# Kernel optimization log

Measured on AMD Instinct MI355X. Metric: run time of the kernel, lower is better.

Reference implementation:

```python
import jax, jax.numpy as jnp
import numpy as np
from jax import lax

B, DIM, H, W = 32, 256, 64, 64
DS = DIM // 4          # dim_split = 64
MLP_H = int(DIM * 2.0)  # mlp_ratio = 2.0
AK = 11                 # att_kernel
EPS = 1e-5


def conv(x, w, b=None, padding=(0, 0), dilation=1, groups=1, stride=1):
    y = lax.conv_general_dilated(
        x, w, (stride, stride),
        [(padding[0], padding[0]), (padding[1], padding[1])],
        rhs_dilation=(dilation, dilation),
        dimension_numbers=('NCHW', 'OIHW', 'NCHW'),
        feature_group_count=groups)
    if b is not None:
        y = y + b[None, :, None, None]
    return y


def bn(x):
    # BatchNorm2d, training-mode batch stats, affine at default init (gamma=1, beta=0)
    m = x.mean(axis=(0, 2, 3), keepdims=True)
    v = ((x - m) ** 2).mean(axis=(0, 2, 3), keepdims=True)
    return (x - m) * lax.rsqrt(v + EPS)


def maxpool2x2(x):
    b, c, h, w = x.shape
    xw = x.reshape(b, c, h // 2, 2, w // 2, 2).transpose(0, 1, 2, 4, 3, 5).reshape(b, c, h // 2, w // 2, 4)
    return xw.max(axis=-1), jnp.argmax(xw, axis=-1)


def maxunpool2x2(y, idx):
    b, c, h, w = y.shape
    oh = jax.nn.one_hot(idx, 4, dtype=y.dtype)  # scatter back into 2x2 window argmax slot
    out = (y[..., None] * oh).reshape(b, c, h, w, 2, 2).transpose(0, 1, 2, 4, 3, 5)
    return out.reshape(b, c, 2 * h, 2 * w)


def maxpool3(x):
    return lax.reduce_window(x, -jnp.inf, lax.max, (1, 1, 3, 3), (1, 1, 1, 1),
                             [(0, 0), (0, 0), (1, 1), (1, 1)])


def blurpool(x):
    # antialiased_cnns.BlurPool(C, stride=3): filt_size=4, reflect pad (1,2)
    f = jnp.array([1., 3., 3., 1.], dtype=x.dtype)
    k = f[:, None] * f[None, :]
    k = k / k.sum()
    c = x.shape[1]
    wgt = jnp.broadcast_to(k[None, None], (c, 1, 4, 4))
    xp = jnp.pad(x, ((0, 0), (0, 0), (1, 2), (1, 2)), mode='reflect')
    return lax.conv_general_dilated(xp, wgt, (3, 3), [(0, 0), (0, 0)],
                                    dimension_numbers=('NCHW', 'OIHW', 'NCHW'),
                                    feature_group_count=c)


def h_tf(x):
    b, c, hh, ww = x.shape
    x = jnp.pad(x, ((0, 0), (0, 0), (0, 0), (0, ww)))
    x = x.reshape(b, c, -1)[..., :-ww]
    return x.reshape(b, c, hh, 2 * ww - 1)


def inv_h_tf(x):
    b, c, hh, _ = x.shape
    x = x.reshape(b, c, -1)
    x = jnp.pad(x, ((0, 0), (0, 0), (0, hh)))
    return x.reshape(b, c, hh, 2 * hh)[..., :hh]


def v_tf(x):
    return h_tf(x.transpose(0, 1, 3, 2)).transpose(0, 1, 3, 2)


def inv_v_tf(x):
    return inv_h_tf(x.transpose(0, 1, 3, 2)).transpose(0, 1, 3, 2)


def ga12(x, p1w, p1b, c0w, c0b, spw, spb, c1w, c1b, c2w, c2b, cw, cb, sqw, sqb, p2w, p2b):
    xp, idx = maxpool2x2(x)
    c = xp.shape[1]
    h = jax.nn.relu(conv(xp, p1w, p1b))
    a1 = conv(h, c0w, c0b, padding=(2, 2), groups=c)                 # depthwise 5x5
    a2 = conv(a1, spw, spb, padding=(9, 9), dilation=3, groups=c)    # depthwise 7x7 dil3
    a1s = conv(a1, c1w, c1b)
    a2s = conv(a2, c2w, c2b)
    comb = jnp.concatenate([a1s, a2s], axis=1)
    agg = jnp.concatenate([comb.mean(axis=1, keepdims=True),
                           comb.max(axis=1, keepdims=True)], axis=1)
    sig = jax.nn.sigmoid(conv(agg, sqw, sqb, padding=(3, 3)))
    attn = conv(a1s * sig[:, 0:1] + a2s * sig[:, 1:2], cw, cb)
    h = conv(h * attn, p2w, p2b)
    return maxunpool2x2(h, idx)


def setup_inputs() -> dict:
    key = jax.random.key(0)
    ks = jax.random.split(key, 32)
    r = lambda i, shape: jax.random.normal(ks[i], shape, jnp.float32) * 0.05
    return {
        'x': jax.random.normal(ks[0], (B, DIM, H, W), jnp.float32),
        'pa_w1': r(1, (4 * DS, DS, 1, 1)),
        'pa_w2': r(2, (DS, 4 * DS, 1, 1)),
        'la_w': r(3, (DS, DS, 3, 3)),
        'mra_h1': r(4, (DS, 1, AK, 3)),
        'mra_v1': r(5, (DS, 1, 3, AK)),
        'mra_h2': r(6, (DS, 1, AK, 3)),
        'mra_v2': r(7, (DS, 1, 3, AK)),
        'g_proj1_w': r(8, (DS, DS, 1, 1)), 'g_proj1_b': r(9, (DS,)),
        'g_conv0_w': r(10, (DS, 1, 5, 5)), 'g_conv0_b': r(11, (DS,)),
        'g_sp_w': r(12, (DS, 1, 7, 7)), 'g_sp_b': r(13, (DS,)),
        'g_c1_w': r(14, (DS // 2, DS, 1, 1)), 'g_c1_b': r(15, (DS // 2,)),
        'g_c2_w': r(16, (DS // 2, DS, 1, 1)), 'g_c2_b': r(17, (DS // 2,)),
        'g_c_w': r(18, (DS, DS // 2, 1, 1)), 'g_c_b': r(19, (DS,)),
        'g_sq_w': r(20, (2, 2, 7, 7)), 'g_sq_b': r(21, (2,)),
        'g_proj2_w': r(22, (DS, DS, 1, 1)), 'g_proj2_b': r(23, (DS,)),
        'mlp_w1': r(24, (MLP_H, DIM, 1, 1)),
        'mlp_w2': r(25, (DIM, MLP_H, 1, 1)),
    }


def reference(x, pa_w1, pa_w2, la_w, mra_h1, mra_v1, mra_h2, mra_v2,
              g_proj1_w, g_proj1_b, g_conv0_w, g_conv0_b, g_sp_w, g_sp_b,
              g_c1_w, g_c1_b, g_c2_w, g_c2_b, g_c_w, g_c_b,
              g_sq_w, g_sq_b, g_proj2_w, g_proj2_b, mlp_w1, mlp_w2):
    x1, x2, x3, x4 = jnp.split(x, 4, axis=1)
    # PA: pixel attention (1x1 expand -> BN -> ReLU -> 1x1) sigmoid gate
    xa1 = x1 * jax.nn.sigmoid(conv(jax.nn.relu(bn(conv(x1, pa_w1))), pa_w2))
    # LA: 3x3 conv -> BN -> ReLU
    xa2 = jax.nn.relu(bn(conv(x2, la_w, padding=(1, 1))))
    # MRA: maxpool3x3 -> blurpool(stride3) -> 4 strip depthwise convs (+diag shear) -> BN -> sigmoid -> nearest upsample gate
    xm = blurpool(maxpool3(x3))
    ph, pv = (AK // 2, 1), (1, AK // 2)
    xh1 = conv(xm, mra_h1, padding=ph, groups=DS)
    xw1 = conv(xm, mra_v1, padding=pv, groups=DS)
    xh2 = inv_h_tf(conv(h_tf(xm), mra_h2, padding=ph, groups=DS))
    xw2 = inv_v_tf(conv(v_tf(xm), mra_v2, padding=pv, groups=DS))
    gate = jax.nn.sigmoid(bn(xh1 + xw1 + xh2 + xw2))
    hs, ws = gate.shape[-2:]
    ri = (jnp.arange(H) * hs) // H   # torch F.interpolate mode='nearest' index rule
    ci = (jnp.arange(W) * ws) // W
    xa3 = x3 * gate[:, :, ri][:, :, :, ci]
    # D_GA (stage==2): maxpool -> GA12 -> BN -> maxunpool
    x4p, idx1 = maxpool2x2(x4)
    xg = ga12(x4p, g_proj1_w, g_proj1_b, g_conv0_w, g_conv0_b, g_sp_w, g_sp_b,
              g_c1_w, g_c1_b, g_c2_w, g_c2_b, g_c_w, g_c_b, g_sq_w, g_sq_b,
              g_proj2_w, g_proj2_b)
    xa4 = maxunpool2x2(bn(xg), idx1)
    x_att = jnp.concatenate([xa1, xa2, xa3, xa4], axis=1)
    # residual MLP (drop_path=0 -> identity)
    return x + conv(jax.nn.relu(bn(conv(x_att, mlp_w1))), mlp_w2)
```

## Files before the change

kernel.cpp:

```cpp
#include <hip/hip_runtime.h>
#include <hip/hip_bf16.h>
#include <math.h>

typedef __hip_bfloat16 bf16;
typedef __attribute__((ext_vector_type(4))) float f32x4;
typedef __attribute__((ext_vector_type(8))) short s16x8;
typedef __attribute__((ext_vector_type(4))) short s16x4;

static __device__ __forceinline__ float bits2f(short s){ return __uint_as_float(((unsigned)(unsigned short)s)<<16); }
static __device__ __forceinline__ short bfbits(float f){ bf16 h = __float2bfloat16(f); return *reinterpret_cast<short*>(&h); }
static __device__ __forceinline__ float ldf(float v){ return v; }
static __device__ __forceinline__ float sigm(float v){ return 1.f/(1.f+__expf(-v)); }

#define P_IMG 4096

#define GLDS16(SRC, DST) __builtin_amdgcn_global_load_lds( \
    (__attribute__((address_space(1))) void*)(SRC), \
    (__attribute__((address_space(3))) void*)(DST), 16, 0, 0)

namespace {
constexpr long long XATT_OFF = 0;
constexpr long long BIG_OFF  = 67108864;
constexpr long long MISC     = 134217728;
constexpr long long XM_OFF   = MISC;
constexpr long long MSUM_OFF = MISC + 3964928;
constexpr long long X4P_OFF  = MISC + 23429120;
constexpr long long IDX1_OFF = MISC + 31817728;
constexpr long long XP_OFF   = MISC + 40206336;
constexpr long long IDX2_OFF = MISC + 42303488;
constexpr long long HBUF_OFF = MISC + 44400640;
constexpr long long A1_OFF   = MISC + 46497792;
constexpr long long A2_OFF   = MISC + 48594944;
constexpr long long A1S_OFF  = MISC + 50692096;
constexpr long long A2S_OFF  = MISC + 51740672;
constexpr long long AGG_OFF  = MISC + 52789248;
constexpr long long SIG_OFF  = MISC + 52854784;
constexpr long long ATTN_OFF = MISC + 52920320;
constexpr long long H2_OFF   = MISC + 55017472;
constexpr long long XG_OFF   = MISC + 57114624;
constexpr long long P33_OFF  = 201326592;
constexpr long long STATS_OFF= 234881024;
constexpr long long WS_NEED  = 234897408;
constexpr long long XPM_OFF  = MISC;
constexpr long long YLA_OFF  = MISC + 33554432;
}

__global__ __launch_bounds__(256) void zero_out_k(float* __restrict__ o, int n){
    int i = blockIdx.x*256 + threadIdx.x;
    if (i < n) o[i] = 0.f;
}

__global__ __launch_bounds__(256) void packw_k(const float* __restrict__ W, short* __restrict__ Wp,
                                               int kshift, int OT16)
{
    int i = blockIdx.x*256 + threadIdx.x;
    int o = i >> kshift;
    int k = i & ((1<<kshift)-1);
    long dest = (((((long)(k>>6)*2 + ((k>>5)&1))*OT16 + (o>>4))*4 + ((k>>3)&3))*16 + (o&15))*8 + (k&7);
    Wp[dest] = bfbits(W[i]);
}

__global__ __launch_bounds__(256) void packw_la_k(const float* __restrict__ W, short* __restrict__ Wp)
{
    int i = blockIdx.x*256 + threadIdx.x;
    int o = i / 576, k = i - o*576;
    int tap = k >> 6, c = k & 63;
    long dest = (((((long)(k>>6)*2 + ((k>>5)&1))*4 + (o>>4))*4 + ((k>>3)&3))*16 + (o&15))*8 + (k&7);
    Wp[dest] = bfbits(W[(o*64 + c)*9 + tap]);
}

__global__ __launch_bounds__(256) void xpose_pm_k(const float* __restrict__ x, short* __restrict__ xpm)
{
    int i = blockIdx.x*256 + threadIdx.x;
    int px = i & 4095, og = (i >> 12) & 15, b = i >> 16;
    s16x8 ov;
    #pragma unroll
    for (int j=0;j<8;j++)
        ov[j] = bfbits(x[((long)b*256 + og*8 + j)*P_IMG + px]);
    *(s16x8*)&xpm[((long)b*P_IMG + px)*128 + og*8] = ov;
}

template<int MT>
__global__ __launch_bounds__(256) void convmfma_dma_k(
    const short* __restrict__ in, int inCtot, int inOff,
    const short* __restrict__ Wp, int K, int OT16,
    short* __restrict__ out, int outC)
{
    static_assert(MT == 4 || MT == 8, "vmcnt counts assume MT in {4,8}");
    __shared__ __align__(16) short sB[2][64*64];
    const int tid = threadIdx.x;
    const int b = blockIdx.z;
    const int Mbase = blockIdx.y * (32*MT);
    const int pxBase = blockIdx.x * 64;
    const int lane = tid & 63, w = tid >> 6;
    const int n16 = lane & 15, q = lane >> 4;
    const int wm = w >> 1, wn = w & 1;
    const int otBase = (Mbase>>4) + wm*MT;

    f32x4 zero = {0.f,0.f,0.f,0.f};
    f32x4 acc[MT][2];
    #pragma unroll
    for (int mt=0;mt<MT;mt++){ acc[mt][0]=zero; acc[mt][1]=zero; }

    const int drow_lo = lane >> 3;
    const int chunk = lane & 7;
    const int seg0 = w*2, seg1 = w*2 + 1;
    const int row0 = seg0*8 + drow_lo, row1 = seg1*8 + drow_lo;
    const int kg0 = chunk ^ (row0 & 7), kg1 = chunk ^ (row1 & 7);
    const short* src0 = in + ((long)b*P_IMG + pxBase + row0)*inCtot + inOff + kg0*8;
    const short* src1 = in + ((long)b*P_IMG + pxBase + row1)*inCtot + inOff + kg1*8;

    const int NT = K >> 6;
    GLDS16(src0, (char*)&sB[0][0] + seg0*1024);
    GLDS16(src1, (char*)&sB[0][0] + seg1*1024);

    for (int t = 0; t < NT; t++){
        const int kb = t << 6;
        s16x8 afr[2][MT];
        #pragma unroll
        for (int kk=0; kk<2; kk++)
            #pragma unroll
            for (int mt=0; mt<MT; mt++)
                afr[kk][mt] = *(const s16x8*)(Wp + ((((long)t*2 + kk)*OT16 + otBase + mt)*64 + lane)*8);
        __builtin_amdgcn_sched_barrier(0);
        if (t+1 < NT){
            GLDS16(src0 + kb + 64, (char*)&sB[(t+1)&1][0] + seg0*1024);
            GLDS16(src1 + kb + 64, (char*)&sB[(t+1)&1][0] + seg1*1024);
            __builtin_amdgcn_sched_barrier(0);
            if constexpr (MT == 8) asm volatile("s_waitcnt vmcnt(18)" ::: "memory");
            else                   asm volatile("s_waitcnt vmcnt(10)" ::: "memory");
        } else {
            __builtin_amdgcn_sched_barrier(0);
            if constexpr (MT == 8) asm volatile("s_waitcnt vmcnt(16)" ::: "memory");
            else                   asm volatile("s_waitcnt vmcnt(8)" ::: "memory");
        }
        __builtin_amdgcn_sched_barrier(0);
        __builtin_amdgcn_s_barrier();
        __builtin_amdgcn_sched_barrier(0);
        const short* sC = &sB[t&1][0];
        #pragma unroll
        for (int kk = 0; kk < 2; kk++){
            s16x8 bfr[2];
            #pragma unroll
            for (int nt=0; nt<2; nt++){
                int n = wn*32 + nt*16 + n16;
                int g = (kk*4 + q) ^ (n & 7);
                bfr[nt] = *(const s16x8*)&sC[n*64 + (g<<3)];
            }
            #pragma unroll
            for (int mt=0; mt<MT; mt++)
                #pragma unroll
                for (int nt=0; nt<2; nt++)
                    acc[mt][nt] = __builtin_amdgcn_mfma_f32_16x16x32_bf16(afr[kk][mt], bfr[nt], acc[mt][nt], 0, 0, 0);
        }
        __builtin_amdgcn_sched_barrier(0);
        __builtin_amdgcn_s_barrier();
        __builtin_amdgcn_sched_barrier(0);
    }

    #pragma unroll
    for (int mt=0; mt<MT; mt++){
        #pragma unroll
        for (int nt=0; nt<2; nt++){
            int px = pxBase + wn*32 + nt*16 + n16;
            int o0 = Mbase + wm*(MT*16) + mt*16 + q*4;
            s16x4 ov;
            #pragma unroll
            for (int r=0; r<4; r++) ov[r] = bfbits(acc[mt][nt][r]);
            *(s16x4*)&out[((long)b*P_IMG + px)*outC + o0] = ov;
        }
    }
}

__global__ __launch_bounds__(256) void la_mfma_k(
    const short* __restrict__ xpm,
    const short* __restrict__ Wp,
    short* __restrict__ y)
{
    __shared__ __align__(16) short sB[2][64*64];
    const int tid = threadIdx.x;
    const int b = blockIdx.z;
    const int hRow = blockIdx.x;
    const int pxBase = hRow*64;
    const int lane = tid & 63, w = tid >> 6;
    const int n16 = lane & 15, q = lane >> 4;
    const int wm = w >> 1, wn = w & 1;
    const int otBase = wm*2;

    f32x4 zero = {0.f,0.f,0.f,0.f};
    f32x4 acc[2][2];
    acc[0][0]=zero; acc[0][1]=zero; acc[1][0]=zero; acc[1][1]=zero;

    const int srow = tid >> 3, schunk = tid & 7;
    const int kgA = schunk ^ (srow & 7);

    auto tapload = [&](int tap, s16x8& v0, s16x8& v1){
        int hh = hRow + (tap/3) - 1;
        int dw = (tap%3) - 1;
        bool hok = (unsigned)hh < 64u;
        s16x8 z = {0,0,0,0,0,0,0,0};
        v0 = z; v1 = z;
        int w0 = srow + dw, w1 = 32 + srow + dw;
        if (hok && (unsigned)w0 < 64u)
            v0 = *(const s16x8*)(xpm + ((long)b*P_IMG + hh*64 + w0)*128 + 64 + kgA*8);
        if (hok && (unsigned)w1 < 64u)
            v1 = *(const s16x8*)(xpm + ((long)b*P_IMG + hh*64 + w1)*128 + 64 + kgA*8);
    };

    s16x8 cv0, cv1;
    tapload(0, cv0, cv1);

    for (int tap = 0; tap < 9; tap++){
        s16x8 nv0 = cv0, nv1 = cv1;
        if (tap+1 < 9) tapload(tap+1, nv0, nv1);
        *(s16x8*)&sB[tap&1][srow*64 + schunk*8]      = cv0;
        *(s16x8*)&sB[tap&1][(32+srow)*64 + schunk*8] = cv1;
        asm volatile("s_waitcnt lgkmcnt(0)" ::: "memory");
        __builtin_amdgcn_sched_barrier(0);
        __builtin_amdgcn_s_barrier();
        __builtin_amdgcn_sched_barrier(0);
        const short* sC = &sB[tap&1][0];
        #pragma unroll
        for (int kk = 0; kk < 2; kk++){
            s16x8 afr[2], bfr[2];
            #pragma unroll
            for (int mt=0; mt<2; mt++)
                afr[mt] = *(const s16x8*)(Wp + ((((long)tap*2 + kk)*4 + otBase + mt)*64 + lane)*8);
            #pragma unroll
            for (int nt=0; nt<2; nt++){
                int n = wn*32 + nt*16 + n16;
                int g = (kk*4 + q) ^ (n & 7);
                bfr[nt] = *(const s16x8*)&sC[n*64 + (g<<3)];
            }
            #pragma unroll
            for (int mt=0; mt<2; mt++)
                #pragma unroll
                for (int nt=0; nt<2; nt++)
                    acc[mt][nt] = __builtin_amdgcn_mfma_f32_16x16x32_bf16(afr[mt], bfr[nt], acc[mt][nt], 0, 0, 0);
        }
        __builtin_amdgcn_sched_barrier(0);
        __builtin_amdgcn_s_barrier();
        __builtin_amdgcn_sched_barrier(0);
        cv0 = nv0; cv1 = nv1;
    }

    #pragma unroll
    for (int mt=0; mt<2; mt++){
        #pragma unroll
        for (int nt=0; nt<2; nt++){
            int px = pxBase + wn*32 + nt*16 + n16;
            int o0 = wm*32 + mt*16 + q*4;
            s16x4 ov;
            #pragma unroll
            for (int r=0; r<4; r++) ov[r] = bfbits(acc[mt][nt][r]);
            *(s16x4*)&y[((long)b*P_IMG + px)*64 + o0] = ov;
        }
    }
}

template<int EPI, typename TOUT, int MT>
__global__ __launch_bounds__(256) void convmfma_reg_k(
    const short* __restrict__ in, int inCtot, int inOff,
    const float2* __restrict__ stats,
    const short* __restrict__ Wp, int K, int OT16,
    TOUT* __restrict__ out, int outC, int outOff,
    const float* __restrict__ aux, int auxC, int auxOff)
{
    __shared__ __align__(16) short sB[2][64*64];
    const int tid = threadIdx.x;
    const int b = blockIdx.z;
    const int Mbase = blockIdx.y * (32*MT);
    const int pxBase = blockIdx.x * 64;
    const int lane = tid & 63, w = tid >> 6;
    const int n16 = lane & 15, q = lane >> 4;
    const int wm = w >> 1, wn = w & 1;
    const int otBase = (Mbase>>4) + wm*MT;

    f32x4 zero = {0.f,0.f,0.f,0.f};
    f32x4 acc[MT][2];
    #pragma unroll
    for (int mt=0;mt<MT;mt++){ acc[mt][0]=zero; acc[mt][1]=zero; }

    const int srow = tid >> 3, schunk = tid & 7;
    const int skg = schunk ^ (srow & 7);
    const short* inrow0 = in + ((long)b*P_IMG + pxBase + srow)*inCtot + inOff + skg*8;
    const short* inrow1 = in + ((long)b*P_IMG + pxBase + 32 + srow)*inCtot + inOff + skg*8;
    const float2* stp = stats + skg*8;

    const int NT = K >> 6;
    s16x8 rv0 = *(const s16x8*)(inrow0);
    s16x8 rv1 = *(const s16x8*)(inrow1);
    const f32x4* sp0 = (const f32x4*)(stp);
    f32x4 p0 = sp0[0], p1 = sp0[1], p2 = sp0[2], p3 = sp0[3];

    for (int t = 0; t < NT; t++){
        const int kb = t << 6;
        s16x8 nrv0 = rv0, nrv1 = rv1;
        f32x4 q0 = p0, q1 = p1, q2 = p2, q3 = p3;
        if (t+1 < NT){
            nrv0 = *(const s16x8*)(inrow0 + kb + 64);
            nrv1 = *(const s16x8*)(inrow1 + kb + 64);
            const f32x4* np = (const f32x4*)(stp + kb + 64);
            q0 = np[0]; q1 = np[1]; q2 = np[2]; q3 = np[3];
        }
        float mm[8] = {p0[0],p0[2],p1[0],p1[2],p2[0],p2[2],p3[0],p3[2]};
        float iv[8] = {p0[1],p0[3],p1[1],p1[3],p2[1],p2[3],p3[1],p3[3]};
        s16x8 sg0, sg1;
        #pragma unroll
        for (int j=0;j<8;j++){
            float f = bits2f(rv0[j]);
            f = (f - mm[j])*iv[j];
            sg0[j] = bfbits(fmaxf(f, 0.f));
        }
        #pragma unroll
        for (int j=0;j<8;j++){
            float f = bits2f(rv1[j]);
            f = (f - mm[j])*iv[j];
            sg1[j] = bfbits(fmaxf(f, 0.f));
        }
        *(s16x8*)&sB[t&1][srow*64 + schunk*8]      = sg0;
        *(s16x8*)&sB[t&1][(32+srow)*64 + schunk*8] = sg1;
        asm volatile("s_waitcnt lgkmcnt(0)" ::: "memory");
        __builtin_amdgcn_sched_barrier(0);
        __builtin_amdgcn_s_barrier();
        __builtin_amdgcn_sched_barrier(0);
        const short* sC = &sB[t&1][0];
        #pragma unroll
        for (int kk = 0; kk < 2; kk++){
            s16x8 afr[MT], bfr[2];
            #pragma unroll
            for (int mt=0; mt<MT; mt++)
                afr[mt] = *(const s16x8*)(Wp + ((((long)t*2 + kk)*OT16 + otBase + mt)*64 + lane)*8);
            #pragma unroll
            for (int nt=0; nt<2; nt++){
                int n = wn*32 + nt*16 + n16;
                int g = (kk*4 + q) ^ (n & 7);
                bfr[nt] = *(const s16x8*)&sC[n*64 + (g<<3)];
            }
            #pragma unroll
            for (int mt=0; mt<MT; mt++)
                #pragma unroll
                for (int nt=0; nt<2; nt++)
                    acc[mt][nt] = __builtin_amdgcn_mfma_f32_16x16x32_bf16(afr[mt], bfr[nt], acc[mt][nt], 0, 0, 0);
        }
        __builtin_amdgcn_sched_barrier(0);
        __builtin_amdgcn_s_barrier();
        __builtin_amdgcn_sched_barrier(0);
        rv0 = nrv0; rv1 = nrv1;
        p0 = q0; p1 = q1; p2 = q2; p3 = q3;
    }

    #pragma unroll
    for (int mt=0; mt<MT; mt++){
        #pragma unroll
        for (int nt=0; nt<2; nt++){
            int px = pxBase + wn*32 + nt*16 + n16;
            int o0 = Mbase + wm*(MT*16) + mt*16 + q*4;
            if constexpr (EPI == 1){
                s16x4 ov;
                #pragma unroll
                for (int r=0; r<4; r++){
                    float av = aux[((long)b*auxC + auxOff + o0 + r)*P_IMG + px];
                    ov[r] = bfbits(av * sigm(acc[mt][nt][r]));
                }
                *(s16x4*)&(((short*)out)[((long)b*P_IMG + px)*outC + outOff + o0]) = ov;
            } else {
                #pragma unroll
                for (int r=0; r<4; r++){
                    int o = o0 + r;
                    float av = aux[((long)b*auxC + auxOff + o)*P_IMG + px];
                    out[((long)b*outC + outOff + o)*P_IMG + px] = av + acc[mt][nt][r];
                }
            }
        }
    }
}

template<int C>
__global__ __launch_bounds__(256) void bnstats_pm_k(const short* __restrict__ in, float* __restrict__ sums)
{
    constexpr int CH8 = C/8;
    constexpr int PL  = 256/CH8;
    __shared__ float accs[2*C];
    const int t = threadIdx.x;
    for (int i=t;i<2*C;i+=256) accs[i]=0.f;
    __syncthreads();
    const int chunk = t & (CH8-1), pl = t / CH8;
    const int b = blockIdx.y;
    float s[8], s2[8];
    #pragma unroll
    for (int j=0;j<8;j++){ s[j]=0.f; s2[j]=0.f; }
    for (int px = blockIdx.x*256 + pl; px < (blockIdx.x+1)*256; px += PL){
        s16x8 v = *(const s16x8*)&in[((long)b*P_IMG + px)*C + chunk*8];
        #pragma unroll
        for (int j=0;j<8;j++){
            float f = bits2f(v[j]);
            s[j] += f; s2[j] = fmaf(f,f,s2[j]);
        }
    }
    #pragma unroll
    for (int j=0;j<8;j++){
        atomicAdd(&accs[(chunk*8+j)*2],   s[j]);
        atomicAdd(&accs[(chunk*8+j)*2+1], s2[j]);
    }
    __syncthreads();
    for (int i=t;i<2*C;i+=256) atomicAdd(&sums[i], accs[i]);
}

template<typename T>
__global__ __launch_bounds__(256) void bnstats_k(const T* __restrict__ in, int Ctot, int cOff, int Pn,
                                                 float* __restrict__ sums)
{
    const int c = blockIdx.x;
    float s=0.f, s2=0.f;
    for (int b=0;b<32;b++){
        const T* qp = in + ((long)b*Ctot + cOff + c)*Pn;
        for (int p = blockIdx.y*256 + threadIdx.x; p < Pn; p += gridDim.y*256){
            float v = ldf(qp[p]);
            s += v; s2 = fmaf(v,v,s2);
        }
    }
    __shared__ float r1[256], r2[256];
    r1[threadIdx.x]=s; r2[threadIdx.x]=s2;
    __syncthreads();
    for (int k=128;k>0;k>>=1){
        if (threadIdx.x<k){ r1[threadIdx.x]+=r1[threadIdx.x+k]; r2[threadIdx.x]+=r2[threadIdx.x+k]; }
        __syncthreads();
    }
    if (threadIdx.x==0){ atomicAdd(&sums[2*c], r1[0]); atomicAdd(&sums[2*c+1], r2[0]); }
}

__global__ __launch_bounds__(256) void bnfin_k(const float* __restrict__ sums, float2* __restrict__ minv,
                                               int C, float invN)
{
    int c = blockIdx.x*256 + threadIdx.x;
    if (c < C){
        float m = sums[2*c]*invN;
        float var = sums[2*c+1]*invN - m*m;
        minv[c] = make_float2(m, 1.f/sqrtf(var + 1e-5f));
    }
}

__global__ __launch_bounds__(256) void la_post_pm_k(const short* __restrict__ y, const float2* __restrict__ minv,
                                                    short* __restrict__ xatt)
{
    int i = blockIdx.x*256 + threadIdx.x;
    int px = i & 4095, og = (i >> 12) & 7, b = i >> 15;
    s16x8 yv = *(const s16x8*)&y[((long)b*P_IMG + px)*64 + og*8];
    s16x8 ov;
    #pragma unroll
    for (int j=0;j<8;j++){
        float2 st = minv[og*8 + j];
        float v = (bits2f(yv[j]) - st.x)*st.y;
        ov[j] = bfbits(fmaxf(v, 0.f));
    }
    *(s16x8*)&xatt[((long)b*P_IMG + px)*256 + 64 + og*8] = ov;
}

__global__ __launch_bounds__(256) void mp3_k(const float* __restrict__ x, float* __restrict__ mp){
    int i = blockIdx.x*256 + threadIdx.x;
    int b = i >> 18, c = (i >> 12) & 63, p = i & 4095;
    int h = p >> 6, wc = p & 63;
    const float* xb = x + ((long)b*256 + 128 + c)*P_IMG;
    float m = -3.4e38f;
    #pragma unroll
    for (int dh=-1; dh<=1; dh++){
        int hh = h+dh; if ((unsigned)hh>=64u) continue;
        #pragma unroll
        for (int dw=-1; dw<=1; dw++){
            int ww = wc+dw; if ((unsigned)ww>=64u) continue;
            m = fmaxf(m, xb[hh*64+ww]);
        }
    }
    mp[i] = m;
}

__global__ __launch_bounds__(256) void blur_k(const float* __restrict__ mp, float* __restrict__ xm){
    int idx = blockIdx.x*256 + threadIdx.x;
    int oj = idx % 22; int t = idx / 22; int oi = t % 22; int bc = t / 22;
    const float* mb = mp + (long)bc * P_IMG;
    const float fw[4] = {1.f,3.f,3.f,1.f};
    float s = 0.f;
    #pragma unroll
    for (int u=0;u<4;u++){
        int r = 3*oi - 1 + u;
        r = r < 0 ? -r : (r > 63 ? 126 - r : r);
        float rs = 0.f;
        #pragma unroll
        for (int v=0; v<4; v++){
            int qq = 3*oj - 1 + v;
            qq = qq < 0 ? -qq : (qq > 63 ? 126 - qq : qq);
            rs = fmaf(fw[v], mb[r*64+qq], rs);
        }
        s = fmaf(fw[u], rs, s);
    }
    xm[idx] = s * (1.f/64.f);
}

__global__ __launch_bounds__(256) void mra_conv_k(const float* __restrict__ xm,
                                                  const float* __restrict__ wh1, const float* __restrict__ wv1,
                                                  const float* __restrict__ wh2, const float* __restrict__ wv2,
                                                  float* __restrict__ msum)
{
    int idx = blockIdx.x*256 + threadIdx.x;
    int j = idx % 22; int t = idx / 22; int i = t % 22; int bc = t / 22; int c = bc & 63;
    const float* xb = xm + (long)bc*484;
    float s = 0.f;
    #pragma unroll
    for (int u=0;u<11;u++){
        int ii = i + u - 5; if ((unsigned)ii >= 22u) continue;
        #pragma unroll
        for (int v=0;v<3;v++){
            int jj = j + v - 1; if ((unsigned)jj >= 22u) continue;
            s = fmaf(wh1[c*33 + u*3 + v], xb[ii*22+jj], s);
        }
    }
    #pragma unroll
    for (int u=0;u<3;u++){
        int ii = i + u - 1; if ((unsigned)ii >= 22u) continue;
        #pragma unroll
        for (int v=0;v<11;v++){
            int jj = j + v - 5; if ((unsigned)jj >= 22u) continue;
            s = fmaf(wv1[c*33 + u*11 + v], xb[ii*22+jj], s);
        }
    }
    {
        int f = i*44 + j; int r = f/43; int q = f - 43*r;
        #pragma unroll
        for (int u=0;u<11;u++){
            int a = r + u - 5; if ((unsigned)a >= 22u) continue;
            #pragma unroll
            for (int v=0;v<3;v++){
                int bcol = q + v - 1; if ((unsigned)bcol >= 43u) continue;
                int g = a*43 + bcol; int rr = g/44; int qq = g - 44*rr;
                if (qq < 22) s = fmaf(wh2[c*33 + u*3 + v], xb[rr*22+qq], s);
            }
        }
    }
    {
        int g = j*44 + i; int r = g/43; int q = g - 43*r;
        #pragma unroll
        for (int u=0;u<3;u++){
            int a = q + u - 1; if ((unsigned)a >= 43u) continue;
            #pragma unroll
            for (int v=0;v<11;v++){
                int bcol = r + v - 5; if ((unsigned)bcol >= 22u) continue;
                int g2 = bcol*43 + a; int rr = g2/44; int qq = g2 - 44*rr;
                if (qq < 22) s = fmaf(wv2[c*33 + u*11 + v], xb[qq*22+rr], s);
            }
        }
    }
    msum[idx] = s;
}

__global__ __launch_bounds__(256) void mra_gate_pm_k(const float* __restrict__ x, const float* __restrict__ msum,
                                                     const float2* __restrict__ minv, short* __restrict__ xatt)
{
    int i = blockIdx.x*256 + threadIdx.x;
    int px = i & 4095, og = (i >> 12) & 7, b = i >> 15;
    int h = px >> 6, wcol = px & 63;
    int ri = (h*22) >> 6, ci = (wcol*22) >> 6;
    s16x8 ov;
    #pragma unroll
    for (int j=0;j<8;j++){
        int c = og*8 + j;
        float g = msum[((long)b*64 + c)*484 + ri*22 + ci];
        float2 st = minv[c];
        g = sigm((g - st.x)*st.y);
        float xv = x[((long)b*256 + 128 + c)*P_IMG + px];
        ov[j] = bfbits(xv * g);
    }
    *(s16x8*)&xatt[((long)b*P_IMG + px)*256 + 128 + og*8] = ov;
}

__global__ __launch_bounds__(256) void pool1_k(const float* __restrict__ x, float* __restrict__ x4p,
                                               int* __restrict__ idx1)
{
    int i = blockIdx.x*256 + threadIdx.x;
    int b = i >> 16, c = (i >> 10) & 63, s = i & 1023;
    int y = s >> 5, xc = s & 31;
    const float* xb = x + ((long)b*256 + 192 + c)*P_IMG;
    float v00 = xb[(2*y)*64 + 2*xc];
    float v01 = xb[(2*y)*64 + 2*xc + 1];
    float v10 = xb[(2*y+1)*64 + 2*xc];
    float v11 = xb[(2*y+1)*64 + 2*xc + 1];
    float best = v00; int bi = 0;
    if (v01 > best){ best = v01; bi = 1; }
    if (v10 > best){ best = v10; bi = 2; }
    if (v11 > best){ best = v11; bi = 3; }
    x4p[i] = best; idx1[i] = bi;
}

__global__ __launch_bounds__(256) void pool2_k(const float* __restrict__ x4p, float* __restrict__ xp,
                                               int* __restrict__ idx2)
{
    int i = blockIdx.x*256 + threadIdx.x;
    int b = i >> 14, c = (i >> 8) & 63, s = i & 255;
    int y = s >> 4, xc = s & 15;
    const float* xb = x4p + ((long)b*64 + c)*1024;
    float v00 = xb[(2*y)*32 + 2*xc];
    float v01 = xb[(2*y)*32 + 2*xc + 1];
    float v10 = xb[(2*y+1)*32 + 2*xc];
    float v11 = xb[(2*y+1)*32 + 2*xc + 1];
    float best = v00; int bi = 0;
    if (v01 > best){ best = v01; bi = 1; }
    if (v10 > best){ best = v10; bi = 2; }
    if (v11 > best){ best = v11; bi = 3; }
    xp[i] = best; idx2[i] = bi;
}

__global__ __launch_bounds__(256) void ga_proj_k(const float* __restrict__ in, const float* __restrict__ mul,
                                                 const float* __restrict__ w, const float* __restrict__ bias,
                                                 float* __restrict__ out, int Cout, int relu)
{
    int s = threadIdx.x, og = blockIdx.x, b = blockIdx.y;
    float acc[8];
    #pragma unroll
    for (int j=0;j<8;j++) acc[j]=0.f;
    for (int c=0;c<64;c++){
        float v = in[((long)b*64 + c)*256 + s];
        if (mul) v *= mul[((long)b*64 + c)*256 + s];
        #pragma unroll
        for (int j=0;j<8;j++) acc[j] = fmaf(v, w[(og*8 + j)*64 + c], acc[j]);
    }
    #pragma unroll
    for (int j=0;j<8;j++){
        int o = og*8 + j;
        float val = acc[j] + bias[o];
        if (relu) val = fmaxf(val, 0.f);
        out[((long)b*Cout + o)*256 + s] = val;
    }
}

__global__ __launch_bounds__(256) void ga_dw5_k(const float* __restrict__ h, const float* __restrict__ w,
                                                const float* __restrict__ bias, float* __restrict__ a1)
{
    int i = blockIdx.x*256 + threadIdx.x;
    int b = i >> 14, c = (i >> 8) & 63, s = i & 255;
    int y = s >> 4, x = s & 15;
    const float* hb = h + ((long)b*64 + c)*256;
    float acc = bias[c];
    #pragma unroll
    for (int u=0;u<5;u++){
        int yy = y + u - 2; if ((unsigned)yy >= 16u) continue;
        #pragma unroll
        for (int v=0;v<5;v++){
            int xx = x + v - 2; if ((unsigned)xx >= 16u) continue;
            acc = fmaf(w[c*25 + u*5 + v], hb[yy*16 + xx], acc);
        }
    }
    a1[i] = acc;
}

__global__ __launch_bounds__(256) void ga_dw7_k(const float* __restrict__ a1, const float* __restrict__ w,
                                                const float* __restrict__ bias, float* __restrict__ a2)
{
    int i = blockIdx.x*256 + threadIdx.x;
    int b = i >> 14, c = (i >> 8) & 63, s = i & 255;
    int y = s >> 4, x = s & 15;
    const float* ab = a1 + ((long)b*64 + c)*256;
    float acc = bias[c];
    #pragma unroll
    for (int u=0;u<7;u++){
        int yy = y + 3*(u-3); if ((unsigned)yy >= 16u) continue;
        #pragma unroll
        for (int v=0;v<7;v++){
            int xx = x + 3*(v-3); if ((unsigned)xx >= 16u) continue;
            acc = fmaf(w[c*49 + u*7 + v], ab[yy*16 + xx], acc);
        }
    }
    a2[i] = acc;
}

__global__ __launch_bounds__(256) void ga_agg_k(const float* __restrict__ a1s, const float* __restrict__ a2s,
                                                float* __restrict__ agg)
{
    int i = blockIdx.x*256 + threadIdx.x;
    int b = i >> 8, s = i & 255;
    float sum = 0.f, mx = -3.4e38f;
    for (int c=0;c<32;c++){
        float v = a1s[((long)b*32 + c)*256 + s];
        sum += v; mx = fmaxf(mx, v);
    }
    for (int c=0;c<32;c++){
        float v = a2s[((long)b*32 + c)*256 + s];
        sum += v; mx = fmaxf(mx, v);
    }
    agg[((long)b*2 + 0)*256 + s] = sum * (1.f/64.f);
    agg[((long)b*2 + 1)*256 + s] = mx;
}

__global__ __launch_bounds__(256) void ga_sq_k(const float* __restrict__ agg, const float* __restrict__ w,
                                               const float* __restrict__ bias, float* __restrict__ sig)
{
    int i = blockIdx.x*256 + threadIdx.x;
    int b = i >> 9, o = (i >> 8) & 1, s = i & 255;
    int y = s >> 4, x = s & 15;
    float acc = bias[o];
    for (int ic=0; ic<2; ic++){
        const float* ab = agg + ((long)b*2 + ic)*256;
        #pragma unroll
        for (int u=0;u<7;u++){
            int yy = y + u - 3; if ((unsigned)yy >= 16u) continue;
            #pragma unroll
            for (int v=0;v<7;v++){
                int xx = x + v - 3; if ((unsigned)xx >= 16u) continue;
                acc = fmaf(w[((o*2 + ic)*7 + u)*7 + v], ab[yy*16 + xx], acc);
            }
        }
    }
    sig[i] = sigm(acc);
}

__global__ __launch_bounds__(256) void ga_attn_k(const float* __restrict__ a1s, const float* __restrict__ a2s,
                                                 const float* __restrict__ sig, const float* __restrict__ w,
                                                 const float* __restrict__ bias, float* __restrict__ attn)
{
    int s = threadIdx.x, og = blockIdx.x, b = blockIdx.y;
    float s0 = sig[((long)b*2 + 0)*256 + s];
    float s1 = sig[((long)b*2 + 1)*256 + s];
    float acc[8];
    #pragma unroll
    for (int j=0;j<8;j++) acc[j]=0.f;
    for (int c=0;c<32;c++){
        float v = a1s[((long)b*32 + c)*256 + s]*s0 + a2s[((long)b*32 + c)*256 + s]*s1;
        #pragma unroll
        for (int j=0;j<8;j++) acc[j] = fmaf(v, w[(og*8 + j)*32 + c], acc[j]);
    }
    #pragma unroll
    for (int j=0;j<8;j++){
        int o = og*8 + j;
        attn[((long)b*64 + o)*256 + s] = acc[j] + bias[o];
    }
}

__global__ __launch_bounds__(256) void ga_unpool1_k(const float* __restrict__ h2, const int* __restrict__ idx2,
                                                    float* __restrict__ xg)
{
    int i = blockIdx.x*256 + threadIdx.x;
    int b = i >> 16, c = (i >> 10) & 63, s = i & 1023;
    int Y = s >> 5, X = s & 31;
    int slot = ((Y & 1) << 1) | (X & 1);
    long pi = ((long)b*64 + c)*256 + (Y >> 1)*16 + (X >> 1);
    xg[i] = (idx2[pi] == slot) ? h2[pi] : 0.f;
}

__global__ __launch_bounds__(256) void ga_out_pm_k(const float* __restrict__ xg, const int* __restrict__ idx1,
                                                   const float2* __restrict__ minv, short* __restrict__ xatt)
{
    int i = blockIdx.x*256 + threadIdx.x;
    int px = i & 4095, og = (i >> 12) & 7, b = i >> 15;
    int hh = px >> 6, ww = px & 63;
    int slot = ((hh & 1) << 1) | (ww & 1);
    s16x8 ov;
    #pragma unroll
    for (int j=0;j<8;j++){
        int c = og*8 + j;
        long pi = ((long)b*64 + c)*1024 + (hh >> 1)*32 + (ww >> 1);
        float v = 0.f;
        if (idx1[pi] == slot){
            float2 st = minv[c];
            v = (xg[pi] - st.x)*st.y;
        }
        ov[j] = bfbits(v);
    }
    *(s16x8*)&xatt[((long)b*P_IMG + px)*256 + 192 + og*8] = ov;
}

extern "C" void kernel_launch(void* const* d_in, const int* in_sizes, int n_in,
                              void* d_out, int out_size, void* d_ws, size_t ws_size,
                              hipStream_t stream)
{
    const float* x      = (const float*)d_in[0];
    const float* pa_w1  = (const float*)d_in[1];
    const float* pa_w2  = (const float*)d_in[2];
    const float* la_w   = (const float*)d_in[3];
    const float* mra_h1 = (const float*)d_in[4];
    const float* mra_v1 = (const float*)d_in[5];
    const float* mra_h2 = (const float*)d_in[6];
    const float* mra_v2 = (const float*)d_in[7];
    const float* g_p1w  = (const float*)d_in[8];
    const float* g_p1b  = (const float*)d_in[9];
    const float* g_c0w  = (const float*)d_in[10];
    const float* g_c0b  = (const float*)d_in[11];
    const float* g_spw  = (const float*)d_in[12];
    const float* g_spb  = (const float*)d_in[13];
    const float* g_c1w  = (const float*)d_in[14];
    const float* g_c1b  = (const float*)d_in[15];
    const float* g_c2w  = (const float*)d_in[16];
    const float* g_c2b  = (const float*)d_in[17];
    const float* g_cw   = (const float*)d_in[18];
    const float* g_cb   = (const float*)d_in[19];
    const float* g_sqw  = (const float*)d_in[20];
    const float* g_sqb  = (const float*)d_in[21];
    const float* g_p2w  = (const float*)d_in[22];
    const float* g_p2b  = (const float*)d_in[23];
    const float* mlp_w1 = (const float*)d_in[24];
    const float* mlp_w2 = (const float*)d_in[25];
    float* outp = (float*)d_out;
    char* ws = (char*)d_ws;

    if (ws_size < (size_t)WS_NEED){
        zero_out_k<<<(out_size + 255)/256, 256, 0, stream>>>(outp, out_size);
        return;
    }

    short* xatt = (short*)(ws + XATT_OFF);
    short* tbuf = (short*)(ws + BIG_OFF);
    short* xpm  = (short*)(ws + XPM_OFF);
    short* yla  = (short*)(ws + YLA_OFF);
    float* xm   = (float*)(ws + XM_OFF);
    float* msum = (float*)(ws + MSUM_OFF);
    float* x4p  = (float*)(ws + X4P_OFF);
    int*   idx1 = (int*)(ws + IDX1_OFF);
    float* xp   = (float*)(ws + XP_OFF);
    int*   idx2 = (int*)(ws + IDX2_OFF);
    float* hbuf = (float*)(ws + HBUF_OFF);
    float* a1   = (float*)(ws + A1_OFF);
    float* a2   = (float*)(ws + A2_OFF);
    float* a1s  = (float*)(ws + A1S_OFF);
    float* a2s  = (float*)(ws + A2S_OFF);
    float* agg  = (float*)(ws + AGG_OFF);
    float* sig  = (float*)(ws + SIG_OFF);
    float* attn = (float*)(ws + ATTN_OFF);
    float* h2   = (float*)(ws + H2_OFF);
    float* xg   = (float*)(ws + XG_OFF);
    float* p33  = (float*)(ws + P33_OFF);
    float* raw  = (float*)(ws + STATS_OFF);
    float*  raw_pa  = raw;
    float*  raw_la  = raw + 512;
    float*  raw_mra = raw + 640;
    float*  raw_ga  = raw + 768;
    float*  raw_mlp = raw + 896;
    float2* mv_pa   = (float2*)(raw + 1920);
    float2* mv_la   = mv_pa + 256;
    float2* mv_mra  = mv_la + 64;
    float2* mv_ga   = mv_mra + 64;
    float2* mv_mlp  = mv_ga + 64;

    hipMemsetAsync(raw, 0, 1920*sizeof(float), stream);

    short* wp_pa1 = (short*)(ws + P33_OFF);
    short* wp_pa2 = wp_pa1 + 256*64;
    short* wp_la  = wp_pa2 + 64*256;
    packw_k<<<64,256,0,stream>>>(pa_w1, wp_pa1, 6, 16);
    packw_k<<<64,256,0,stream>>>(pa_w2, wp_pa2, 8, 4);
    packw_la_k<<<144,256,0,stream>>>(la_w, wp_la);

    xpose_pm_k<<<8192,256,0,stream>>>(x, xpm);

    convmfma_dma_k<8><<<dim3(64,1,32),256,0,stream>>>(xpm,128,0, wp_pa1,64,16, tbuf,256);
    bnstats_pm_k<256><<<dim3(16,32),256,0,stream>>>(tbuf, raw_pa);
    bnfin_k<<<1,256,0,stream>>>(raw_pa, mv_pa, 256, 1.f/131072.f);
    convmfma_reg_k<1,short,2><<<dim3(64,1,32),256,0,stream>>>(tbuf,256,0, mv_pa, wp_pa2,256,4,
                                                              xatt,256,0, x,256,0);

    la_mfma_k<<<dim3(64,1,32),256,0,stream>>>(xpm, wp_la, yla);
    bnstats_pm_k<64><<<dim3(16,32),256,0,stream>>>(yla, raw_la);
    bnfin_k<<<1,256,0,stream>>>(raw_la, mv_la, 64, 1.f/131072.f);
    la_post_pm_k<<<4096,256,0,stream>>>(yla, mv_la, xatt);

    mp3_k<<<32768,256,0,stream>>>(x, p33);
    blur_k<<<3872,256,0,stream>>>(p33, xm);
    mra_conv_k<<<3872,256,0,stream>>>(xm, mra_h1, mra_v1, mra_h2, mra_v2, msum);
    bnstats_k<float><<<dim3(64,2),256,0,stream>>>(msum,64,0,484, raw_mra);
    bnfin_k<<<1,256,0,stream>>>(raw_mra, mv_mra, 64, 1.f/15488.f);
    mra_gate_pm_k<<<4096,256,0,stream>>>(x, msum, mv_mra, xatt);

    pool1_k<<<8192,256,0,stream>>>(x, x4p, idx1);
    pool2_k<<<2048,256,0,stream>>>(x4p, xp, idx2);
    ga_proj_k<<<dim3(8,32),256,0,stream>>>(xp, nullptr, g_p1w, g_p1b, hbuf, 64, 1);
    ga_dw5_k<<<2048,256,0,stream>>>(hbuf, g_c0w, g_c0b, a1);
    ga_dw7_k<<<2048,256,0,stream>>>(a1, g_spw, g_spb, a2);
    ga_proj_k<<<dim3(4,32),256,0,stream>>>(a1, nullptr, g_c1w, g_c1b, a1s, 32, 0);
    ga_proj_k<<<dim3(4,32),256,0,stream>>>(a2, nullptr, g_c2w, g_c2b, a2s, 32, 0);
    ga_agg_k<<<32,256,0,stream>>>(a1s, a2s, agg);
    ga_sq_k<<<64,256,0,stream>>>(agg, g_sqw, g_sqb, sig);
    ga_attn_k<<<dim3(8,32),256,0,stream>>>(a1s, a2s, sig, g_cw, g_cb, attn);
    ga_proj_k<<<dim3(8,32),256,0,stream>>>(hbuf, attn, g_p2w, g_p2b, h2, 64, 0);
    ga_unpool1_k<<<8192,256,0,stream>>>(h2, idx2, xg);
    bnstats_k<float><<<dim3(64,4),256,0,stream>>>(xg,64,0,1024, raw_ga);
    bnfin_k<<<1,256,0,stream>>>(raw_ga, mv_ga, 64, 1.f/32768.f);
    ga_out_pm_k<<<4096,256,0,stream>>>(xg, idx1, mv_ga, xatt);

    short* wm1 = (short*)(ws + P33_OFF);
    short* wm2 = wm1 + 512*256;
    packw_k<<<512,256,0,stream>>>(mlp_w1, wm1, 8, 32);
    packw_k<<<512,256,0,stream>>>(mlp_w2, wm2, 9, 16);
    convmfma_dma_k<8><<<dim3(64,2,32),256,0,stream>>>(xatt,256,0, wm1,256,32, tbuf,512);
    bnstats_pm_k<512><<<dim3(16,32),256,0,stream>>>(tbuf, raw_mlp);
    bnfin_k<<<2,256,0,stream>>>(raw_mlp, mv_mlp, 512, 1.f/131072.f);
    convmfma_reg_k<2,float,8><<<dim3(64,1,32),256,0,stream>>>(tbuf,512,0, mv_mlp, wm2,512,16,
                                                              outp,256,0, x,256,0);
}
```

Baseline: 973.4 us.

## Fuse BatchNorm statistics into MFMA conv epilogues and retile final MLP conv

Computes per-channel sum and sum-of-squares of conv outputs directly from accumulator registers in the conv kernels, using lane shuffles, LDS atomics, then global atomics. This removes three separate bnstats passes that re-read large bf16 intermediates from memory. Stats now come from fp32 accumulators rather than bf16-rounded stored values, which slightly changes numerics. The final MLP conv also switches to MT=4 with twice the grid in y, giving more blocks for occupancy.

```diff
diff --git a/kernel.cpp b/kernel.cpp
--- a/kernel.cpp
+++ b/kernel.cpp
@@ -80,14 +80,15 @@
     *(s16x8*)&xpm[((long)b*P_IMG + px)*128 + og*8] = ov;
 }
 
-template<int MT>
+template<int MT, bool STATS>
 __global__ __launch_bounds__(256) void convmfma_dma_k(
     const short* __restrict__ in, int inCtot, int inOff,
     const short* __restrict__ Wp, int K, int OT16,
-    short* __restrict__ out, int outC)
+    short* __restrict__ out, int outC, float* __restrict__ sums)
 {
     static_assert(MT == 4 || MT == 8, "vmcnt counts assume MT in {4,8}");
     __shared__ __align__(16) short sB[2][64*64];
+    __shared__ float sAccs[STATS ? 64*MT : 1];
     const int tid = threadIdx.x;
     const int b = blockIdx.z;
     const int Mbase = blockIdx.y * (32*MT);
@@ -170,14 +171,42 @@
             *(s16x4*)&out[((long)b*P_IMG + px)*outC + o0] = ov;
         }
     }
+
+    if constexpr (STATS){
+        for (int i=tid; i<64*MT; i+=256) sAccs[i] = 0.f;
+        __syncthreads();
+        #pragma unroll
+        for (int mt=0; mt<MT; mt++){
+            #pragma unroll
+            for (int r=0; r<4; r++){
+                float s  = acc[mt][0][r] + acc[mt][1][r];
+                float s2 = acc[mt][0][r]*acc[mt][0][r] + acc[mt][1][r]*acc[mt][1][r];
+                #pragma unroll
+                for (int d=1; d<16; d<<=1){
+                    s  += __shfl_xor(s,  d);
+                    s2 += __shfl_xor(s2, d);
+                }
+                if (n16 == 0){
+                    int rel = wm*(MT*16) + mt*16 + q*4 + r;
+                    atomicAdd(&sAccs[2*rel],   s);
+                    atomicAdd(&sAccs[2*rel+1], s2);
+                }
+            }
+        }
+        __syncthreads();
+        for (int i=tid; i<64*MT; i+=256)
+            atomicAdd(&sums[2*Mbase + i], sAccs[i]);
+    }
 }
 
 __global__ __launch_bounds__(256) void la_mfma_k(
     const short* __restrict__ xpm,
     const short* __restrict__ Wp,
-    short* __restrict__ y)
+    short* __restrict__ y,
+    float* __restrict__ sums)
 {
     __shared__ __align__(16) short sB[2][64*64];
+    __shared__ float sAccs[128];
     const int tid = threadIdx.x;
     const int b = blockIdx.z;
     const int hRow = blockIdx.x;
@@ -256,6 +285,29 @@
             *(s16x4*)&y[((long)b*P_IMG + px)*64 + o0] = ov;
         }
     }
+
+    for (int i=tid; i<128; i+=256) sAccs[i] = 0.f;
+    __syncthreads();
+    #pragma unroll
+    for (int mt=0; mt<2; mt++){
+        #pragma unroll
+        for (int r=0; r<4; r++){
+            float s  = acc[mt][0][r] + acc[mt][1][r];
+            float s2 = acc[mt][0][r]*acc[mt][0][r] + acc[mt][1][r]*acc[mt][1][r];
+            #pragma unroll
+            for (int d=1; d<16; d<<=1){
+                s  += __shfl_xor(s,  d);
+                s2 += __shfl_xor(s2, d);
+            }
+            if (n16 == 0){
+                int rel = wm*32 + mt*16 + q*4 + r;
+                atomicAdd(&sAccs[2*rel],   s);
+                atomicAdd(&sAccs[2*rel+1], s2);
+            }
+        }
+    }
+    __syncthreads();
+    if (tid < 128) atomicAdd(&sums[tid], sAccs[tid]);
 }
 
 template<int EPI, typename TOUT, int MT>
@@ -374,37 +426,6 @@
             }
         }
     }
-}
-
-template<int C>
-__global__ __launch_bounds__(256) void bnstats_pm_k(const short* __restrict__ in, float* __restrict__ sums)
-{
-    constexpr int CH8 = C/8;
-    constexpr int PL  = 256/CH8;
-    __shared__ float accs[2*C];
-    const int t = threadIdx.x;
-    for (int i=t;i<2*C;i+=256) accs[i]=0.f;
-    __syncthreads();
-    const int chunk = t & (CH8-1), pl = t / CH8;
-    const int b = blockIdx.y;
-    float s[8], s2[8];
-    #pragma unroll
-    for (int j=0;j<8;j++){ s[j]=0.f; s2[j]=0.f; }
-    for (int px = blockIdx.x*256 + pl; px < (blockIdx.x+1)*256; px += PL){
-        s16x8 v = *(const s16x8*)&in[((long)b*P_IMG + px)*C + chunk*8];
-        #pragma unroll
-        for (int j=0;j<8;j++){
-            float f = bits2f(v[j]);
-            s[j] += f; s2[j] = fmaf(f,f,s2[j]);
-        }
-    }
-    #pragma unroll
-    for (int j=0;j<8;j++){
-        atomicAdd(&accs[(chunk*8+j)*2],   s[j]);
-        atomicAdd(&accs[(chunk*8+j)*2+1], s2[j]);
-    }
-    __syncthreads();
-    for (int i=t;i<2*C;i+=256) atomicAdd(&sums[i], accs[i]);
 }
 
 template<typename T>
@@ -849,14 +870,12 @@
 
     xpose_pm_k<<<8192,256,0,stream>>>(x, xpm);
 
-    convmfma_dma_k<8><<<dim3(64,1,32),256,0,stream>>>(xpm,128,0, wp_pa1,64,16, tbuf,256);
-    bnstats_pm_k<256><<<dim3(16,32),256,0,stream>>>(tbuf, raw_pa);
+    convmfma_dma_k<8,true><<<dim3(64,1,32),256,0,stream>>>(xpm,128,0, wp_pa1,64,16, tbuf,256, raw_pa);
     bnfin_k<<<1,256,0,stream>>>(raw_pa, mv_pa, 256, 1.f/131072.f);
     convmfma_reg_k<1,short,2><<<dim3(64,1,32),256,0,stream>>>(tbuf,256,0, mv_pa, wp_pa2,256,4,
                                                               xatt,256,0, x,256,0);
 
-    la_mfma_k<<<dim3(64,1,32),256,0,stream>>>(xpm, wp_la, yla);
-    bnstats_pm_k<64><<<dim3(16,32),256,0,stream>>>(yla, raw_la);
+    la_mfma_k<<<dim3(64,1,32),256,0,stream>>>(xpm, wp_la, yla, raw_la);
     bnfin_k<<<1,256,0,stream>>>(raw_la, mv_la, 64, 1.f/131072.f);
     la_post_pm_k<<<4096,256,0,stream>>>(yla, mv_la, xatt);
 
@@ -887,9 +906,8 @@
     short* wm2 = wm1 + 512*256;
     packw_k<<<512,256,0,stream>>>(mlp_w1, wm1, 8, 32);
     packw_k<<<512,256,0,stream>>>(mlp_w2, wm2, 9, 16);
-    convmfma_dma_k<8><<<dim3(64,2,32),256,0,stream>>>(xatt,256,0, wm1,256,32, tbuf,512);
-    bnstats_pm_k<512><<<dim3(16,32),256,0,stream>>>(tbuf, raw_mlp);
+    convmfma_dma_k<8,true><<<dim3(64,2,32),256,0,stream>>>(xatt,256,0, wm1,256,32, tbuf,512, raw_mlp);
     bnfin_k<<<2,256,0,stream>>>(raw_mlp, mv_mlp, 512, 1.f/131072.f);
-    convmfma_reg_k<2,float,8><<<dim3(64,1,32),256,0,stream>>>(tbuf,512,0, mv_mlp, wm2,512,16,
+    convmfma_reg_k<2,float,4><<<dim3(64,2,32),256,0,stream>>>(tbuf,512,0, mv_mlp, wm2,512,16,
                                                               outp,256,0, x,256,0);
 }
```

Measured after the change: 976.0 us. Within noise of the previous version (+0.3%).
